# Optimization experiments

Hardware: AMD Instinct MI355X
Metric: run time of the kernel (lower is better)

Reference implementation:

```python
import jax, jax.numpy as jnp
import numpy as np

NUM_HEADS = 8
HEAD_DIM = 64
LATENT = NUM_HEADS * HEAD_DIM  # 512
IN_CH = 256


def setup_inputs() -> dict:
    key = jax.random.key(0)
    k1, k2, k3, k4 = jax.random.split(key, 4)
    b, c, h, w = 16, IN_CH, 64, 64
    net = jax.random.normal(k1, (b, c, h, w), dtype=jnp.float32)
    # 1x1 conv weights (out_ch, in_ch); scaled like kaiming-ish init
    w_qkv = jax.random.normal(k2, (3 * LATENT, c), dtype=jnp.float32) / np.sqrt(c)
    w_out = jax.random.normal(k3, (c, LATENT), dtype=jnp.float32) / np.sqrt(LATENT)
    b_out = jax.random.normal(k4, (c,), dtype=jnp.float32) * 0.01
    return {"net": net, "w_qkv": w_qkv, "w_out": w_out, "b_out": b_out}


def reference(net, w_qkv, w_out, b_out):
    b, c, h, w = net.shape
    n = h * w
    # 1x1 conv == channel GEMM: (b, 3L, n)
    qkv = jnp.einsum("bchw,oc->bohw", net, w_qkv).reshape(b, 3, NUM_HEADS, HEAD_DIM, n)
    q, k, v = qkv[:, 0], qkv[:, 1], qkv[:, 2]  # each (b, H, D, n)
    k = jax.nn.softmax(k, axis=-1)  # softmax over spatial tokens
    context = jnp.einsum("bhdn,bhen->bhde", k, v)  # (b, H, D, D)
    out = jnp.einsum("bhde,bhdn->bhen", context, q)  # (b, H, D, n)
    out = out.reshape(b, LATENT, h, w)
    # output 1x1 conv with bias
    out = jnp.einsum("blhw,cl->bchw", out, w_out) + b_out[None, :, None, None]
    return out
```

## Files before the change

kernel.cpp:

```cpp
#include <hip/hip_runtime.h>


typedef unsigned short u16;
typedef unsigned int u32;
typedef __attribute__((ext_vector_type(4))) u16 u16x4;
typedef __attribute__((ext_vector_type(4))) u32 u32x4;
typedef __attribute__((ext_vector_type(4))) float f32x4;
typedef __attribute__((ext_vector_type(8))) short bf16x8;

__device__ __forceinline__ u16 f2bf(float f) {
  union { float f; u32 u; } x; x.f = f;
  u32 r = x.u + 0x7fffu + ((x.u >> 16) & 1u);
  return (u16)(r >> 16);
}

__device__ __forceinline__ void async16(const u16* g, u16* l) {
  __builtin_amdgcn_global_load_lds(
      (const __attribute__((address_space(1))) void*)g,
      (__attribute__((address_space(3))) void*)l, 16, 0, 0);
}

__global__ __launch_bounds__(256) void cast_w(const float* __restrict__ w,
                                              u16* __restrict__ o) {
  int i = (blockIdx.x * 256 + threadIdx.x) * 4;
  f32x4 v = *(const f32x4*)(w + i);
  u16x4 u;
  u[0] = f2bf(v[0]); u[1] = f2bf(v[1]); u[2] = f2bf(v[2]); u[3] = f2bf(v[3]);
  *(u16x4*)(o + i) = u;
}

__global__ __launch_bounds__(256) void transpose_cast_g(const float* __restrict__ in,
                                                        u16* __restrict__ out,
                                                        int R, int C) {
  __shared__ float t[64][65];
  const int b = blockIdx.z, r0 = blockIdx.y * 64, c0 = blockIdx.x * 64;
  const float* ip = in + (size_t)b * R * C;
  u16* op = out + (size_t)b * R * C;
  const int tid = threadIdx.x;
  const int col4 = (tid & 15) * 4, rr0 = tid >> 4;
#pragma unroll
  for (int i = 0; i < 4; ++i) {
    int r = rr0 + i * 16;
    f32x4 v = *(const f32x4*)(ip + (size_t)(r0 + r) * C + c0 + col4);
    t[r][col4 + 0] = v[0]; t[r][col4 + 1] = v[1];
    t[r][col4 + 2] = v[2]; t[r][col4 + 3] = v[3];
  }
  __syncthreads();
  const int cc4 = (tid & 15) * 4, nr0 = tid >> 4;
#pragma unroll
  for (int i = 0; i < 4; ++i) {
    int nr = nr0 + i * 16;
    u16x4 u;
    u[0] = f2bf(t[cc4 + 0][nr]); u[1] = f2bf(t[cc4 + 1][nr]);
    u[2] = f2bf(t[cc4 + 2][nr]); u[3] = f2bf(t[cc4 + 3][nr]);
    *(u16x4*)(op + (size_t)(c0 + nr) * R + r0 + cc4) = u;
  }
}

__global__ __launch_bounds__(512, 4) void kv_ctx_fused(
    const u16* __restrict__ wkv,
    const u16* __restrict__ netT,
    float* __restrict__ ctxp,
    float* __restrict__ sump) {
  __shared__ __align__(16) u16 Bs[2][8192];
  __shared__ __align__(16) u16 ekL[2048];
  __shared__ __align__(16) u16 vL[2048];

  const int flat = blockIdx.x;
  const int xcd = flat & 7, inner = flat >> 3;
  const int b = 2 * xcd + (inner >> 5);
  const int h = (inner >> 2) & 7;
  const int s = inner & 3;

  const int tid = threadIdx.x, lane = tid & 63, wid = tid >> 6;
  const int wq = wid & 3, wn = wid >> 2;
  const int lr = lane & 15, lg = lane >> 4;
  const bool isK = (wq < 2);

  bf16x8 af[2][8];
#pragma unroll
  for (int mi = 0; mi < 2; ++mi) {
    const int r = wq * 32 + mi * 16 + lr;
    const int grow = (r < 64) ? h * 64 + r : 512 + h * 64 + (r - 64);
#pragma unroll
    for (int kk = 0; kk < 8; ++kk)
      af[mi][kk] = *(const bf16x8*)(wkv + (size_t)grow * 256 + kk * 32 + lg * 8);
  }

  const u16* Bsrc = netT + ((size_t)b * 4096 + s * 1024) * 256;
  const int srow = tid >> 5;
  const int sslot = tid & 31;
  auto stage = [&](int c, int buf) {
    const u16* src = Bsrc + (size_t)c * 32 * 256;
#pragma unroll
    for (int i = 0; i < 2; ++i) {
      const int row = i * 16 + srow;
      const int scol = ((sslot ^ (row & 7)) * 8);
      async16(src + row * 256 + scol, &Bs[buf][i * 4096 + tid * 8]);
    }
  };

  f32x4 cacc[2] = {};
  f32x4 sacc = {};
  bf16x8 ones8;
#pragma unroll
  for (int j = 0; j < 8; ++j) ((u16*)&ones8)[j] = 0x3F80;

  auto ctx_acc = [&]() {
    const int d = wq * 16 + lr;
    bf16x8 ekf = *(const bf16x8*)&ekL[d * 32 + ((lg ^ (d & 3)) * 8)];
#pragma unroll
    for (int ei = 0; ei < 2; ++ei) {
      const int e = wn * 32 + ei * 16 + lr;
      bf16x8 vf = *(const bf16x8*)&vL[e * 32 + ((lg ^ (e & 3)) * 8)];
      cacc[ei] = __builtin_amdgcn_mfma_f32_16x16x32_bf16(ekf, vf, cacc[ei], 0, 0, 0);
    }
    if (wn == 0)
      sacc = __builtin_amdgcn_mfma_f32_16x16x32_bf16(ekf, ones8, sacc, 0, 0, 0);
  };

  stage(0, 0);
  asm volatile("s_waitcnt vmcnt(0)" ::: "memory");
  __syncthreads();

  for (int c = 0; c < 32; ++c) {
    const int p = c & 1;
    if (c + 1 < 32) {
      stage(c + 1, p ^ 1);
      asm volatile("s_waitcnt vmcnt(2)" ::: "memory");
    } else {
      asm volatile("s_waitcnt vmcnt(0)" ::: "memory");
    }
    __syncthreads();

    f32x4 kvacc[2] = {};
    __builtin_amdgcn_s_setprio(1);
    if (c > 0) ctx_acc();
    const int nrow = wn * 16 + lr;
#pragma unroll
    for (int kk = 0; kk < 8; ++kk) {
      bf16x8 bfr = *(const bf16x8*)&Bs[p][nrow * 256 + (((kk * 4 + lg) ^ (nrow & 7)) * 8)];
      kvacc[0] = __builtin_amdgcn_mfma_f32_16x16x32_bf16(af[0][kk], bfr, kvacc[0], 0, 0, 0);
      kvacc[1] = __builtin_amdgcn_mfma_f32_16x16x32_bf16(af[1][kk], bfr, kvacc[1], 0, 0, 0);
    }
    __builtin_amdgcn_s_setprio(0);
    __syncthreads();

    u16* dstL = isK ? ekL : vL;
#pragma unroll
    for (int mi = 0; mi < 2; ++mi)
#pragma unroll
      for (int j = 0; j < 4; ++j) {
        float v = kvacc[mi][j];
        if (isK) v = __expf(v);
        const u32 u = __float_as_uint(v);
        const u16 bv = (u16)((u + 0x8000u) >> 16);
        const int dd = (wq & 1) * 32 + mi * 16 + lg * 4 + j;
        const int n = wn * 16 + lr;
        dstL[dd * 32 + (((n >> 3) ^ (dd & 3)) * 8) + (n & 7)] = bv;
      }
  }
  __syncthreads();
  ctx_acc();

  float* cp = ctxp + (((size_t)(b * 8 + h) * 4 + s) * 4096);
#pragma unroll
  for (int ei = 0; ei < 2; ++ei)
#pragma unroll
    for (int j = 0; j < 4; ++j) {
      const int d = wq * 16 + lg * 4 + j;
      const int e = wn * 32 + ei * 16 + lr;
      cp[d * 64 + e] = cacc[ei][j];
    }
  if (wn == 0 && lr == 0) {
#pragma unroll
    for (int j = 0; j < 4; ++j)
      sump[((size_t)(b * 8 + h) * 4 + s) * 64 + wq * 16 + lg * 4 + j] = sacc[j];
  }
}

__global__ __launch_bounds__(256) void fold_w2(const float* __restrict__ ctxp,
                                               const float* __restrict__ sump,
                                               const float* __restrict__ wout,
                                               u16* __restrict__ W2) {
  __shared__ float cl[16 * 64];
  __shared__ float sl[16];
  const int bh = blockIdx.x, dq = blockIdx.y;
  const int b = bh >> 3, h = bh & 7;
  const int tid = threadIdx.x;
  f32x4 v4 = {0.f, 0.f, 0.f, 0.f};
#pragma unroll
  for (int ch = 0; ch < 4; ++ch)
    v4 += *(const f32x4*)(ctxp + ((size_t)bh * 4 + ch) * 4096 + dq * 1024 + tid * 4);
  *(f32x4*)&cl[tid * 4] = v4;
  if (tid < 16) {
    float ss = 0.f;
#pragma unroll
    for (int ch = 0; ch < 4; ++ch)
      ss += sump[((size_t)bh * 4 + ch) * 64 + dq * 16 + tid];
    sl[tid] = ss;
  }
  __syncthreads();
  const int c = tid;
  f32x4 wv[16];
  const float* wrow = wout + (size_t)c * 512 + h * 64;
#pragma unroll
  for (int i = 0; i < 16; ++i) wv[i] = *(const f32x4*)(wrow + i * 4);
#pragma unroll
  for (int d = 0; d < 16; ++d) {
    f32x4 s4 = {0.f, 0.f, 0.f, 0.f};
#pragma unroll
    for (int e4 = 0; e4 < 16; ++e4) {
      f32x4 cv = *(const f32x4*)&cl[d * 64 + e4 * 4];
      s4 += wv[e4] * cv;
    }
    const float s = (s4[0] + s4[1] + s4[2] + s4[3]) / sl[d];
    W2[((size_t)b * 256 + c) * 512 + h * 64 + dq * 16 + d] = f2bf(s);
  }
}

template <int LD, int NK, int MODE>
__global__ __launch_bounds__(256) void gemm128(const u16* __restrict__ A,
                                               const u16* __restrict__ B,
                                               size_t aStride, size_t bStride,
                                               void* __restrict__ O0,
                                               const float* __restrict__ bias) {
  __shared__ __align__(16) u16 SM[32768];
  const int b = blockIdx.z, mt = blockIdx.y, nt = blockIdx.x;
  const int tid = threadIdx.x, lane = tid & 63, wid = tid >> 6;
  const int wr = wid >> 1, wc = wid & 1, lr = lane & 15, lg = lane >> 4;
  const u16* Ap = A + (size_t)b * aStride + (size_t)mt * 128 * LD;
  const u16* Bp = B + (size_t)b * bStride + (size_t)nt * 128 * LD;

  auto stage = [&](int buf, int ks) {
    const int k0 = ks * 64;
#pragma unroll
    for (int i = 0; i < 4; ++i) {
      const int idx = i * 2048 + tid * 8;
      const int r = idx >> 6, c = idx & 63;
      async16(Ap + (size_t)r * LD + k0 + c, SM + buf * 8192 + i * 2048 + wid * 512);
      async16(Bp + (size_t)r * LD + k0 + c, SM + 16384 + buf * 8192 + i * 2048 + wid * 512);
    }
  };

  f32x4 acc[4][4] = {};
  stage(0, 0);
  asm volatile("s_waitcnt vmcnt(0)" ::: "memory");
  __syncthreads();
  for (int ks = 0; ks < NK; ++ks) {
    const int buf = ks & 1;
    if (ks + 1 < NK) stage(buf ^ 1, ks + 1);
    const u16* Ab = SM + buf * 8192;
    const u16* Bb = SM + 16384 + buf * 8192;
#pragma unroll
    for (int kk = 0; kk < 2; ++kk) {
      bf16x8 afm[4], bfr[4];
#pragma unroll
      for (int mi = 0; mi < 4; ++mi)
        afm[mi] = *(const bf16x8*)(Ab + (wr * 64 + mi * 16 + lr) * 64 + kk * 32 + lg * 8);
#pragma unroll
      for (int ni = 0; ni < 4; ++ni)
        bfr[ni] = *(const bf16x8*)(Bb + (wc * 64 + ni * 16 + lr) * 64 + kk * 32 + lg * 8);
#pragma unroll
      for (int mi = 0; mi < 4; ++mi)
#pragma unroll
        for (int ni = 0; ni < 4; ++ni)
          acc[mi][ni] = __builtin_amdgcn_mfma_f32_16x16x32_bf16(afm[mi], bfr[ni], acc[mi][ni], 0, 0, 0);
    }
    asm volatile("s_waitcnt vmcnt(0)" ::: "memory");
    __syncthreads();
  }

  if constexpr (MODE == 2) {
    u16* Cs = SM;
#pragma unroll
    for (int mi = 0; mi < 4; ++mi)
#pragma unroll
      for (int ni = 0; ni < 4; ++ni)
#pragma unroll
        for (int j = 0; j < 4; ++j)
          Cs[(wr * 64 + mi * 16 + lg * 4 + j) * 128 + wc * 64 + ni * 16 + lr] =
              f2bf(acc[mi][ni][j]);
    __syncthreads();
    u16* dst = (u16*)O0;
#pragma unroll
    for (int p = 0; p < 8; ++p) {
      const int idx = p * 2048 + tid * 8;
      const int r = idx >> 7, cc = idx & 127;
      *(u32x4*)(dst + ((size_t)b * 256 + mt * 128 + r) * 256 + nt * 128 + cc) =
          *(const u32x4*)(Cs + idx);
    }
  } else {
    float* Cf = (float*)SM;
#pragma unroll
    for (int mi = 0; mi < 4; ++mi)
#pragma unroll
      for (int ni = 0; ni < 4; ++ni)
#pragma unroll
        for (int j = 0; j < 4; ++j) {
          const int row = wr * 64 + mi * 16 + lg * 4 + j;
          Cf[row * 128 + wc * 64 + ni * 16 + lr] = acc[mi][ni][j] + bias[mt * 128 + row];
        }
    __syncthreads();
    float* op = (float*)O0;
#pragma unroll
    for (int p = 0; p < 16; ++p) {
      const int idx = p * 1024 + tid * 4;
      const int r = idx >> 7, cc = idx & 127;
      *(f32x4*)(op + ((size_t)b * 256 + mt * 128 + r) * 4096 + nt * 128 + cc) =
          *(const f32x4*)(Cf + idx);
    }
  }
}

extern "C" void kernel_launch(void* const* d_in, const int* in_sizes, int n_in,
                              void* d_out, int out_size, void* d_ws, size_t ws_size,
                              hipStream_t stream) {
  const float* net  = (const float*)d_in[0];
  const float* wqkv = (const float*)d_in[1];
  const float* wout = (const float*)d_in[2];
  const float* bout = (const float*)d_in[3];
  float* out = (float*)d_out;

  char* ws = (char*)d_ws;
  u16*   netT = (u16*)(ws + 0);
  float* ctxp = (float*)(ws + 33554432);
  float* sump = (float*)(ws + 41943040);
  u16*   W2   = (u16*)(ws + 42074112);
  u16*   W3   = (u16*)(ws + 46268416);
  u16*   wkv  = (u16*)(ws + 48365568);
  u16*   wqTb = (u16*)(ws + 48889856);

  cast_w<<<256, 256, 0, stream>>>(wqkv + 512 * 256, wkv);
  transpose_cast_g<<<dim3(64, 4, 16), 256, 0, stream>>>(net, netT, 256, 4096);
  transpose_cast_g<<<dim3(4, 8, 1), 256, 0, stream>>>(wqkv, wqTb, 512, 256);
  kv_ctx_fused<<<512, 512, 0, stream>>>(wkv, netT, ctxp, sump);
  fold_w2<<<dim3(128, 4), 256, 0, stream>>>(ctxp, sump, wout, W2);
  gemm128<512, 8, 2><<<dim3(2, 2, 16), 256, 0, stream>>>(
      W2, wqTb, (size_t)256 * 512, 0, W3, nullptr);
  gemm128<256, 4, 1><<<dim3(32, 2, 16), 256, 0, stream>>>(
      W3, netT, (size_t)256 * 256, (size_t)4096 * 256, out, bout);
}
```

Baseline: 117.1 us.

## Triple-buffer B tiles and double-buffer ek/v to drop one barrier per chunk

The kv_ctx_fused loop now stages B tiles two chunks ahead in a three-slot buffer and double-buffers the ek/v LDS tiles, which removes the second __syncthreads per iteration. It uses raw s_barrier with explicit waitcnts. It also splits the MFMA K loop into two independent accumulator chains to shorten dependency latency, and changes the LDS swizzle to reduce bank conflicts on the ek/v writes. The cost is more LDS per block (about 56KB vs 40KB), which may reduce how many blocks fit on a CU.

```diff
diff --git a/kernel.cpp b/kernel.cpp
--- a/kernel.cpp
+++ b/kernel.cpp
@@ -62,9 +62,9 @@
     const u16* __restrict__ netT,
     float* __restrict__ ctxp,
     float* __restrict__ sump) {
-  __shared__ __align__(16) u16 Bs[2][8192];
-  __shared__ __align__(16) u16 ekL[2048];
-  __shared__ __align__(16) u16 vL[2048];
+  __shared__ __align__(16) u16 Bs[3][8192];
+  __shared__ __align__(16) u16 ekL[2][2048];
+  __shared__ __align__(16) u16 vL[2][2048];
 
   const int flat = blockIdx.x;
   const int xcd = flat & 7, inner = flat >> 3;
@@ -106,13 +106,15 @@
 #pragma unroll
   for (int j = 0; j < 8; ++j) ((u16*)&ones8)[j] = 0x3F80;
 
-  auto ctx_acc = [&]() {
+  auto ctx_acc = [&](int p) {
     const int d = wq * 16 + lr;
-    bf16x8 ekf = *(const bf16x8*)&ekL[d * 32 + ((lg ^ (d & 3)) * 8)];
+    const int Fd = ((d >> 2) ^ d) & 3;
+    bf16x8 ekf = *(const bf16x8*)&ekL[p][d * 32 + (((lg ^ Fd) & 3) * 8)];
 #pragma unroll
     for (int ei = 0; ei < 2; ++ei) {
       const int e = wn * 32 + ei * 16 + lr;
-      bf16x8 vf = *(const bf16x8*)&vL[e * 32 + ((lg ^ (e & 3)) * 8)];
+      const int Fe = ((e >> 2) ^ e) & 3;
+      bf16x8 vf = *(const bf16x8*)&vL[p][e * 32 + (((lg ^ Fe) & 3) * 8)];
       cacc[ei] = __builtin_amdgcn_mfma_f32_16x16x32_bf16(ekf, vf, cacc[ei], 0, 0, 0);
     }
     if (wn == 0)
@@ -120,48 +122,58 @@
   };
 
   stage(0, 0);
-  asm volatile("s_waitcnt vmcnt(0)" ::: "memory");
-  __syncthreads();
+  stage(1, 1);
+  const int nrow = wn * 16 + lr;
 
   for (int c = 0; c < 32; ++c) {
-    const int p = c & 1;
-    if (c + 1 < 32) {
-      stage(c + 1, p ^ 1);
-      asm volatile("s_waitcnt vmcnt(2)" ::: "memory");
+    if (c < 31) {
+      asm volatile("s_waitcnt vmcnt(2) lgkmcnt(0)" ::: "memory");
     } else {
-      asm volatile("s_waitcnt vmcnt(0)" ::: "memory");
-    }
-    __syncthreads();
-
-    f32x4 kvacc[2] = {};
+      asm volatile("s_waitcnt vmcnt(0) lgkmcnt(0)" ::: "memory");
+    }
+    __builtin_amdgcn_s_barrier();
+    asm volatile("" ::: "memory");
+
+    if (c + 2 < 32) stage(c + 2, (c + 2) % 3);
+
+    const u16* Bb = Bs[c % 3];
+    f32x4 kvA[2] = {}, kvB[2] = {};
     __builtin_amdgcn_s_setprio(1);
-    if (c > 0) ctx_acc();
-    const int nrow = wn * 16 + lr;
-#pragma unroll
-    for (int kk = 0; kk < 8; ++kk) {
-      bf16x8 bfr = *(const bf16x8*)&Bs[p][nrow * 256 + (((kk * 4 + lg) ^ (nrow & 7)) * 8)];
-      kvacc[0] = __builtin_amdgcn_mfma_f32_16x16x32_bf16(af[0][kk], bfr, kvacc[0], 0, 0, 0);
-      kvacc[1] = __builtin_amdgcn_mfma_f32_16x16x32_bf16(af[1][kk], bfr, kvacc[1], 0, 0, 0);
+    if (c > 0) ctx_acc((c - 1) & 1);
+#pragma unroll
+    for (int kk = 0; kk < 4; ++kk) {
+      bf16x8 bfr = *(const bf16x8*)&Bb[nrow * 256 + (((kk * 4 + lg) ^ (nrow & 7)) * 8)];
+      kvA[0] = __builtin_amdgcn_mfma_f32_16x16x32_bf16(af[0][kk], bfr, kvA[0], 0, 0, 0);
+      kvA[1] = __builtin_amdgcn_mfma_f32_16x16x32_bf16(af[1][kk], bfr, kvA[1], 0, 0, 0);
+    }
+#pragma unroll
+    for (int kk = 4; kk < 8; ++kk) {
+      bf16x8 bfr = *(const bf16x8*)&Bb[nrow * 256 + (((kk * 4 + lg) ^ (nrow & 7)) * 8)];
+      kvB[0] = __builtin_amdgcn_mfma_f32_16x16x32_bf16(af[0][kk], bfr, kvB[0], 0, 0, 0);
+      kvB[1] = __builtin_amdgcn_mfma_f32_16x16x32_bf16(af[1][kk], bfr, kvB[1], 0, 0, 0);
     }
     __builtin_amdgcn_s_setprio(0);
-    __syncthreads();
-
-    u16* dstL = isK ? ekL : vL;
-#pragma unroll
-    for (int mi = 0; mi < 2; ++mi)
+
+    u16* dstL = isK ? ekL[c & 1] : vL[c & 1];
+#pragma unroll
+    for (int mi = 0; mi < 2; ++mi) {
+      f32x4 kv4 = kvA[mi] + kvB[mi];
 #pragma unroll
       for (int j = 0; j < 4; ++j) {
-        float v = kvacc[mi][j];
+        float v = kv4[j];
         if (isK) v = __expf(v);
         const u32 u = __float_as_uint(v);
         const u16 bv = (u16)((u + 0x8000u) >> 16);
         const int dd = (wq & 1) * 32 + mi * 16 + lg * 4 + j;
-        const int n = wn * 16 + lr;
-        dstL[dd * 32 + (((n >> 3) ^ (dd & 3)) * 8) + (n & 7)] = bv;
+        const int F = ((dd >> 2) ^ dd) & 3;
+        dstL[dd * 32 + ((((nrow >> 3) ^ F) & 3) * 8) + (nrow & 7)] = bv;
       }
-  }
-  __syncthreads();
-  ctx_acc();
+    }
+  }
+  asm volatile("s_waitcnt lgkmcnt(0)" ::: "memory");
+  __builtin_amdgcn_s_barrier();
+  asm volatile("" ::: "memory");
+  ctx_acc(1);
 
   float* cp = ctxp + (((size_t)(b * 8 + h) * 4 + s) * 4096);
 #pragma unroll
```

After: 131.6 us. +12.4%, slower.

## Double-buffer ekL/vL in kv_ctx_fused and XCD-swizzle final GEMM blocks

Applied to the files above, without the earlier changes.

In the fused K/V-context kernel, the exp(K) and V tiles in LDS become double-buffered. This drops one barrier per chunk and moves the next-chunk async stage to after the top barrier, so each chunk's context MFMA reads the previous buffer while the current buffer is written. The final output GEMM now uses a flat 1D grid that maps blocks to batches by XCD, so the netT tiles of a batch stay in one XCD's L2. The price is extra LDS for the duplicated buffers, and the reordered waits now depend on the implicit vmcnt drain at the barrier for correctness.

```diff
diff --git a/kernel.cpp b/kernel.cpp
--- a/kernel.cpp
+++ b/kernel.cpp
@@ -63,8 +63,8 @@
     float* __restrict__ ctxp,
     float* __restrict__ sump) {
   __shared__ __align__(16) u16 Bs[2][8192];
-  __shared__ __align__(16) u16 ekL[2048];
-  __shared__ __align__(16) u16 vL[2048];
+  __shared__ __align__(16) u16 ekL[2][2048];
+  __shared__ __align__(16) u16 vL[2][2048];
 
   const int flat = blockIdx.x;
   const int xcd = flat & 7, inner = flat >> 3;
@@ -106,13 +106,13 @@
 #pragma unroll
   for (int j = 0; j < 8; ++j) ((u16*)&ones8)[j] = 0x3F80;
 
-  auto ctx_acc = [&]() {
+  auto ctx_acc = [&](int q) {
     const int d = wq * 16 + lr;
-    bf16x8 ekf = *(const bf16x8*)&ekL[d * 32 + ((lg ^ (d & 3)) * 8)];
+    bf16x8 ekf = *(const bf16x8*)&ekL[q][d * 32 + ((lg ^ (d & 3)) * 8)];
 #pragma unroll
     for (int ei = 0; ei < 2; ++ei) {
       const int e = wn * 32 + ei * 16 + lr;
-      bf16x8 vf = *(const bf16x8*)&vL[e * 32 + ((lg ^ (e & 3)) * 8)];
+      bf16x8 vf = *(const bf16x8*)&vL[q][e * 32 + ((lg ^ (e & 3)) * 8)];
       cacc[ei] = __builtin_amdgcn_mfma_f32_16x16x32_bf16(ekf, vf, cacc[ei], 0, 0, 0);
     }
     if (wn == 0)
@@ -120,23 +120,16 @@
   };
 
   stage(0, 0);
-  asm volatile("s_waitcnt vmcnt(0)" ::: "memory");
-  __syncthreads();
+  const int nrow = wn * 16 + lr;
 
   for (int c = 0; c < 32; ++c) {
     const int p = c & 1;
-    if (c + 1 < 32) {
-      stage(c + 1, p ^ 1);
-      asm volatile("s_waitcnt vmcnt(2)" ::: "memory");
-    } else {
-      asm volatile("s_waitcnt vmcnt(0)" ::: "memory");
-    }
     __syncthreads();
+    if (c + 1 < 32) stage(c + 1, p ^ 1);
 
     f32x4 kvacc[2] = {};
     __builtin_amdgcn_s_setprio(1);
-    if (c > 0) ctx_acc();
-    const int nrow = wn * 16 + lr;
+    if (c > 0) ctx_acc(p ^ 1);
 #pragma unroll
     for (int kk = 0; kk < 8; ++kk) {
       bf16x8 bfr = *(const bf16x8*)&Bs[p][nrow * 256 + (((kk * 4 + lg) ^ (nrow & 7)) * 8)];
@@ -144,9 +137,8 @@
       kvacc[1] = __builtin_amdgcn_mfma_f32_16x16x32_bf16(af[1][kk], bfr, kvacc[1], 0, 0, 0);
     }
     __builtin_amdgcn_s_setprio(0);
-    __syncthreads();
-
-    u16* dstL = isK ? ekL : vL;
+
+    u16* dstL = isK ? ekL[p] : vL[p];
 #pragma unroll
     for (int mi = 0; mi < 2; ++mi)
 #pragma unroll
@@ -156,12 +148,11 @@
         const u32 u = __float_as_uint(v);
         const u16 bv = (u16)((u + 0x8000u) >> 16);
         const int dd = (wq & 1) * 32 + mi * 16 + lg * 4 + j;
-        const int n = wn * 16 + lr;
-        dstL[dd * 32 + (((n >> 3) ^ (dd & 3)) * 8) + (n & 7)] = bv;
+        dstL[dd * 32 + (((nrow >> 3) ^ (dd & 3)) * 8) + (nrow & 7)] = bv;
       }
   }
   __syncthreads();
-  ctx_acc();
+  ctx_acc(1);
 
   float* cp = ctxp + (((size_t)(b * 8 + h) * 4 + s) * 4096);
 #pragma unroll
@@ -226,7 +217,16 @@
                                                void* __restrict__ O0,
                                                const float* __restrict__ bias) {
   __shared__ __align__(16) u16 SM[32768];
-  const int b = blockIdx.z, mt = blockIdx.y, nt = blockIdx.x;
+  int b, mt, nt;
+  if constexpr (MODE == 1) {
+    const int flat = blockIdx.x;
+    const int xcd = flat & 7, r = flat >> 3;
+    b = 2 * xcd + (r >> 6);
+    nt = (r & 63) >> 1;
+    mt = r & 1;
+  } else {
+    b = blockIdx.z; mt = blockIdx.y; nt = blockIdx.x;
+  }
   const int tid = threadIdx.x, lane = tid & 63, wid = tid >> 6;
   const int wr = wid >> 1, wc = wid & 1, lr = lane & 15, lg = lane >> 4;
   const u16* Ap = A + (size_t)b * aStride + (size_t)mt * 128 * LD;
@@ -237,9 +237,9 @@
 #pragma unroll
     for (int i = 0; i < 4; ++i) {
       const int idx = i * 2048 + tid * 8;
-      const int r = idx >> 6, c = idx & 63;
-      async16(Ap + (size_t)r * LD + k0 + c, SM + buf * 8192 + i * 2048 + wid * 512);
-      async16(Bp + (size_t)r * LD + k0 + c, SM + 16384 + buf * 8192 + i * 2048 + wid * 512);
+      const int r2 = idx >> 6, c2 = idx & 63;
+      async16(Ap + (size_t)r2 * LD + k0 + c2, SM + buf * 8192 + i * 2048 + wid * 512);
+      async16(Bp + (size_t)r2 * LD + k0 + c2, SM + 16384 + buf * 8192 + i * 2048 + wid * 512);
     }
   };
 
@@ -286,8 +286,8 @@
 #pragma unroll
     for (int p = 0; p < 8; ++p) {
       const int idx = p * 2048 + tid * 8;
-      const int r = idx >> 7, cc = idx & 127;
-      *(u32x4*)(dst + ((size_t)b * 256 + mt * 128 + r) * 256 + nt * 128 + cc) =
+      const int r2 = idx >> 7, cc = idx & 127;
+      *(u32x4*)(dst + ((size_t)b * 256 + mt * 128 + r2) * 256 + nt * 128 + cc) =
           *(const u32x4*)(Cs + idx);
     }
   } else {
@@ -306,8 +306,8 @@
 #pragma unroll
     for (int p = 0; p < 16; ++p) {
       const int idx = p * 1024 + tid * 4;
-      const int r = idx >> 7, cc = idx & 127;
-      *(f32x4*)(op + ((size_t)b * 256 + mt * 128 + r) * 4096 + nt * 128 + cc) =
+      const int r2 = idx >> 7, cc = idx & 127;
+      *(f32x4*)(op + ((size_t)b * 256 + mt * 128 + r2) * 4096 + nt * 128 + cc) =
           *(const f32x4*)(Cf + idx);
     }
   }
@@ -338,6 +338,6 @@
   fold_w2<<<dim3(128, 4), 256, 0, stream>>>(ctxp, sump, wout, W2);
   gemm128<512, 8, 2><<<dim3(2, 2, 16), 256, 0, stream>>>(
       W2, wqTb, (size_t)256 * 512, 0, W3, nullptr);
-  gemm128<256, 4, 1><<<dim3(32, 2, 16), 256, 0, stream>>>(
+  gemm128<256, 4, 1><<<dim3(1024, 1, 1), 256, 0, stream>>>(
       W3, netT, (size_t)256 * 256, (size_t)4096 * 256, out, bout);
 }
```

Measured after the change: 113.9 us (median of 3 runs). 1.03x faster.
